# Kernel tuning notes

Measured on AMD Instinct MI355X. Metric: run time of the kernel, lower is better.

## Reference

```python
import jax, jax.numpy as jnp
import numpy as np

N = 50000
E = 600000
F_IN = 128
DIM = 128
BN_EPS = 1e-5


def _batchnorm(x, gamma, beta):
    # training-mode BatchNorm1d: biased batch stats over node dim
    mean = jnp.mean(x, axis=0)
    var = jnp.var(x, axis=0)
    return (x - mean) * jax.lax.rsqrt(var + BN_EPS) * gamma + beta


def _gin_layer(x, src, dst, Wa, ba, Wb, bb):
    # GINConv with eps=0: h_i = MLP(x_i + sum_{j->i} x_j)
    agg = jax.ops.segment_sum(x[src], dst, num_segments=N)
    h = x + agg
    h = jnp.maximum(h @ Wa + ba, 0.0) @ Wb + bb
    return h


def setup_inputs() -> dict:
    key = jax.random.key(0)
    ks = jax.random.split(key, 16)

    def lin(k, fan_in, fan_out):
        bound = 1.0 / np.sqrt(fan_in)
        kw, kb = jax.random.split(k)
        W = jax.random.uniform(kw, (fan_in, fan_out), jnp.float32, -bound, bound)
        b = jax.random.uniform(kb, (fan_out,), jnp.float32, -bound, bound)
        return W, b

    x = jax.random.normal(ks[0], (N, F_IN), jnp.float32)
    edge_index = jax.random.randint(ks[1], (2, E), 0, N, jnp.int64)

    W1a, b1a = lin(ks[2], F_IN, DIM)
    W1b, b1b = lin(ks[3], DIM, DIM)
    W2a, b2a = lin(ks[4], DIM, DIM)
    W2b, b2b = lin(ks[5], DIM, DIM)
    W5a, b5a = lin(ks[6], DIM, DIM)
    W5b, b5b = lin(ks[7], DIM, 2)

    g1 = jnp.ones((DIM,), jnp.float32); be1 = jnp.zeros((DIM,), jnp.float32)
    g2 = jnp.ones((DIM,), jnp.float32); be2 = jnp.zeros((DIM,), jnp.float32)
    g5 = jnp.ones((2,), jnp.float32); be5 = jnp.zeros((2,), jnp.float32)

    return dict(x=x, edge_index=edge_index,
                W1a=W1a, b1a=b1a, W1b=W1b, b1b=b1b, g1=g1, be1=be1,
                W2a=W2a, b2a=b2a, W2b=W2b, b2b=b2b, g2=g2, be2=be2,
                W5a=W5a, b5a=b5a, W5b=W5b, b5b=b5b, g5=g5, be5=be5)


def reference(x, edge_index,
              W1a, b1a, W1b, b1b, g1, be1,
              W2a, b2a, W2b, b2b, g2, be2,
              W5a, b5a, W5b, b5b, g5, be5):
    src, dst = edge_index[0], edge_index[1]
    h = jnp.maximum(_gin_layer(x, src, dst, W1a, b1a, W1b, b1b), 0.0)
    h = _batchnorm(h, g1, be1)
    h = jnp.maximum(_gin_layer(h, src, dst, W2a, b2a, W2b, b2b), 0.0)
    h = _batchnorm(h, g2, be2)
    h = jnp.maximum(_gin_layer(h, src, dst, W5a, b5a, W5b, b5b), 0.0)
    h = _batchnorm(h, g5, be5)
    return h
```

## Files before the change

kernel.cpp:

```cpp
#include <hip/hip_runtime.h>


constexpr int Nn = 50000;
constexpr int Ne = 600000;

typedef __attribute__((ext_vector_type(8))) short short8;
typedef __attribute__((ext_vector_type(4))) float f32x4;

__device__ inline float bflo(uint u) { return __uint_as_float(u << 16); }
__device__ inline float bfhi(uint u) { return __uint_as_float(u & 0xffff0000u); }
__device__ inline ushort f2b(float f) {
  uint x = __float_as_uint(f);
  return (ushort)((x + 0x7fffu + ((x >> 16) & 1u)) >> 16);
}
__device__ inline uint pack2(float a, float b) {
  return (uint)f2b(a) | ((uint)f2b(b) << 16);
}

constexpr int CVT_B = (Nn * 32) / 256;
constexpr int PK_B = (5 * 2048) / 256;
constexpr int EH_B = (Ne + 255) / 256;
__global__ __launch_bounds__(256) void prep_all(
    const float4* __restrict__ x4, uint2* __restrict__ xb,
    const float* __restrict__ Wa, const float* __restrict__ Wb,
    const float* __restrict__ Wc, const float* __restrict__ Wd,
    const float* __restrict__ We, ushort* __restrict__ pw,
    const int* __restrict__ dst, int* __restrict__ rp) {
  int b = blockIdx.x;
  if (b < CVT_B) {
    int i = b * 256 + threadIdx.x;
    float4 v = x4[i];
    xb[i] = make_uint2(pack2(v.x, v.y), pack2(v.z, v.w));
  } else if (b < CVT_B + PK_B) {
    int t = (b - CVT_B) * 256 + threadIdx.x;
    int mat = t >> 11;
    int r = t & 2047;
    int lane = r & 63;
    int ktnt = r >> 6;
    int kt = ktnt & 3, nt = ktnt >> 2;
    const float* W = mat == 0 ? Wa : mat == 1 ? Wb : mat == 2 ? Wc : mat == 3 ? Wd : We;
    int c = nt * 16 + (lane & 15);
    int k0 = kt * 32 + 8 * (lane >> 4);
    ushort tmp[8];
#pragma unroll
    for (int j = 0; j < 8; j++) tmp[j] = f2b(W[(size_t)(k0 + j) * 128 + c]);
    *(uint4*)&pw[(size_t)mat * 16384 + r * 8] = *(uint4*)tmp;
  } else {
    int e = (b - CVT_B - PK_B) * 256 + threadIdx.x;
    if (e < Ne) atomicAdd(&rp[dst[e] + 1], 1);
  }
}

constexpr int SCAN_N = Nn + 1;
constexpr int SCAN_G = (SCAN_N + 1023) / 1024;

__global__ __launch_bounds__(1024) void scan_p1(int* __restrict__ rp,
                                                int* __restrict__ bsum) {
  __shared__ int wsum[16];
  __shared__ int wpre[16];
  int i = blockIdx.x * 1024 + threadIdx.x;
  int lane = threadIdx.x & 63, wv = threadIdx.x >> 6;
  int v = (i < SCAN_N) ? rp[i] : 0;
#pragma unroll
  for (int off = 1; off < 64; off <<= 1) {
    int t = __shfl_up(v, off);
    if (lane >= off) v += t;
  }
  if (lane == 63) wsum[wv] = v;
  __syncthreads();
  if (threadIdx.x == 0) {
    int acc = 0;
#pragma unroll
    for (int w = 0; w < 16; w++) {
      wpre[w] = acc;
      acc += wsum[w];
    }
    bsum[blockIdx.x] = acc;
  }
  __syncthreads();
  if (i < SCAN_N) rp[i] = v + wpre[wv];
}

__global__ void scan_p2(int* __restrict__ bsum) {
  if (threadIdx.x == 0 && blockIdx.x == 0) {
    int acc = 0;
    for (int b = 0; b < SCAN_G; b++) {
      int t = bsum[b];
      bsum[b] = acc;
      acc += t;
    }
  }
}

__global__ __launch_bounds__(1024) void scan_p3(int* __restrict__ rp,
                                                const int* __restrict__ bsum,
                                                int* __restrict__ cur) {
  int i = blockIdx.x * 1024 + threadIdx.x;
  if (i < SCAN_N) {
    int v = rp[i] + bsum[blockIdx.x];
    rp[i] = v;
    if (i < Nn) cur[i] = v;
  }
}

__global__ __launch_bounds__(256) void edge_fill(const int* __restrict__ src,
                                                 const int* __restrict__ dst,
                                                 int* __restrict__ cur,
                                                 int* __restrict__ cols) {
  int e = blockIdx.x * 256 + threadIdx.x;
  if (e < Ne) {
    int p = atomicAdd(&cur[dst[e]], 1);
    cols[p] = src[e];
  }
}

template <bool FOLD>
__global__ __launch_bounds__(256) void gather_bn(const uint* __restrict__ X,
                                                 const int* __restrict__ rp,
                                                 const int* __restrict__ cols,
                                                 const float* __restrict__ sums,
                                                 const float* __restrict__ gamma,
                                                 const float* __restrict__ beta,
                                                 uint* __restrict__ H) {
  int wid = (blockIdx.x * 256 + threadIdx.x) >> 6;
  if (wid >= Nn) return;
  int lane = threadIdx.x & 63;
  int f0 = lane * 2;
  float A0 = 1.f, A1 = 1.f, B0 = 0.f, B1 = 0.f;
  if (FOLD) {
    float m0 = sums[f0] * (1.f / Nn), m1 = sums[f0 + 1] * (1.f / Nn);
    float v0 = sums[128 + f0] * (1.f / Nn) - m0 * m0;
    float v1 = sums[128 + f0 + 1] * (1.f / Nn) - m1 * m1;
    A0 = rsqrtf(v0 + 1e-5f) * gamma[f0];
    A1 = rsqrtf(v1 + 1e-5f) * gamma[f0 + 1];
    B0 = beta[f0] - m0 * A0;
    B1 = beta[f0 + 1] - m1 * A1;
  }
  int p0 = rp[wid], p1 = rp[wid + 1];
  int deg = p1 - p0;
  uint su = X[(size_t)wid * 64 + lane];
  float ax = bflo(su), ay = bfhi(su);
  if (deg > 0) {
    int ci = p0 + (lane & 31);
    int cv = cols[ci < p1 ? ci : p1 - 1];
    if (deg <= 16) {
#pragma unroll
      for (int j = 0; j < 16; j++) {
        int s = __shfl(cv, j);
        uint u = X[(size_t)s * 64 + lane];
        float m = j < deg ? 1.f : 0.f;
        ax = fmaf(m, bflo(u), ax);
        ay = fmaf(m, bfhi(u), ay);
      }
    } else {
#pragma unroll
      for (int j = 0; j < 32; j++) {
        int s = __shfl(cv, j);
        uint u = X[(size_t)s * 64 + lane];
        float m = j < deg ? 1.f : 0.f;
        ax = fmaf(m, bflo(u), ax);
        ay = fmaf(m, bfhi(u), ay);
      }
      for (int p = p0 + 32; p < p1; ++p) {
        int s = __builtin_amdgcn_readfirstlane(cols[p]);
        uint u = X[(size_t)s * 64 + lane];
        ax += bflo(u);
        ay += bfhi(u);
      }
    }
  }
  float cnt = (float)(deg + 1);
  float ox = FOLD ? A0 * ax + cnt * B0 : ax;
  float oy = FOLD ? A1 * ay + cnt * B1 : ay;
  H[(size_t)wid * 64 + lane] = pack2(ox, oy);
}

constexpr int MLP_ROWS = 128;
__global__ __launch_bounds__(256, 2) void gin_mlp(const ushort* __restrict__ A,
                                                  const uint4* __restrict__ pWa,
                                                  const float* __restrict__ ba,
                                                  const short8* __restrict__ pWb,
                                                  const float* __restrict__ bb,
                                                  ushort* __restrict__ C,
                                                  float* __restrict__ stats) {
  __shared__ uint4 W1l[2048];
  __shared__ ushort T[64][136];
  __shared__ float sS[128], sQ[128];
  int tid = threadIdx.x;
#pragma unroll
  for (int i = 0; i < 8; i++) W1l[tid + i * 256] = pWa[tid + i * 256];
  if (tid < 128) {
    sS[tid] = 0.f;
    sQ[tid] = 0.f;
  }
  int wv = tid >> 6, l = tid & 63, lr = l & 15, lg = l >> 4;
  int rowb = wv * 16 + lr;
  int row0 = blockIdx.x * MLP_ROWS;

  short8 w2r[8][4];
#pragma unroll
  for (int nt = 0; nt < 8; nt++)
#pragma unroll
    for (int kt = 0; kt < 4; kt++) w2r[nt][kt] = pWb[(nt * 4 + kt) * 64 + l];
  __builtin_amdgcn_sched_barrier(0);
  __syncthreads();

  for (int rt = 0; rt < MLP_ROWS / 64; rt++) {
    int row = row0 + rt * 64 + rowb;
    bool ok = row < Nn;

    short8 afr[4];
#pragma unroll
    for (int kt = 0; kt < 4; kt++) {
      afr[kt] = short8{};
      if (ok) afr[kt] = *(const short8*)(A + (size_t)row * 128 + kt * 32 + lg * 8);
    }
    f32x4 acc[8];
#pragma unroll
    for (int nt = 0; nt < 8; nt++) {
      float4 bv = *(const float4*)&ba[nt * 16 + lg * 4];
      acc[nt][0] = bv.x; acc[nt][1] = bv.y; acc[nt][2] = bv.z; acc[nt][3] = bv.w;
    }
#pragma unroll
    for (int kt = 0; kt < 4; kt++)
#pragma unroll
      for (int nt = 0; nt < 8; nt++) {
        short8 w1 = *(const short8*)&W1l[(nt * 4 + kt) * 64 + l];
        acc[nt] = __builtin_amdgcn_mfma_f32_16x16x32_bf16(w1, afr[kt], acc[nt],
                                                          0, 0, 0);
      }
#pragma unroll
    for (int nt = 0; nt < 8; nt++) {
      float v0 = fmaxf(acc[nt][0], 0.f), v1 = fmaxf(acc[nt][1], 0.f);
      float v2 = fmaxf(acc[nt][2], 0.f), v3 = fmaxf(acc[nt][3], 0.f);
      *(uint2*)&T[rowb][nt * 16 + lg * 4] = make_uint2(pack2(v0, v1), pack2(v2, v3));
    }
    __syncthreads();

    short8 tfr[4];
#pragma unroll
    for (int kt = 0; kt < 4; kt++) tfr[kt] = *(const short8*)&T[rowb][kt * 32 + lg * 8];
    f32x4 acc2[8];
#pragma unroll
    for (int nt = 0; nt < 8; nt++) {
      float4 bv = *(const float4*)&bb[nt * 16 + lg * 4];
      acc2[nt][0] = bv.x; acc2[nt][1] = bv.y; acc2[nt][2] = bv.z; acc2[nt][3] = bv.w;
    }
#pragma unroll
    for (int kt = 0; kt < 4; kt++)
#pragma unroll
      for (int nt = 0; nt < 8; nt++)
        acc2[nt] = __builtin_amdgcn_mfma_f32_16x16x32_bf16(w2r[nt][kt], tfr[kt],
                                                           acc2[nt], 0, 0, 0);

#pragma unroll
    for (int nt = 0; nt < 8; nt++) {
      float v[4];
#pragma unroll
      for (int r = 0; r < 4; r++) v[r] = fmaxf(acc2[nt][r], 0.f);
      if (ok)
        *(uint2*)&C[(size_t)row * 128 + nt * 16 + lg * 4] =
            make_uint2(pack2(v[0], v[1]), pack2(v[2], v[3]));
#pragma unroll
      for (int r = 0; r < 4; r++) {
        float s_ = ok ? v[r] : 0.f;
        float q_ = s_ * s_;
        s_ += __shfl_xor(s_, 1);  q_ += __shfl_xor(q_, 1);
        s_ += __shfl_xor(s_, 2);  q_ += __shfl_xor(q_, 2);
        s_ += __shfl_xor(s_, 4);  q_ += __shfl_xor(q_, 4);
        s_ += __shfl_xor(s_, 8);  q_ += __shfl_xor(q_, 8);
        if (lr == 0) {
          atomicAdd(&sS[nt * 16 + lg * 4 + r], s_);
          atomicAdd(&sQ[nt * 16 + lg * 4 + r], q_);
        }
      }
    }
    __syncthreads();
  }
  if (tid < 128) {
    atomicAdd(&stats[tid], sS[tid]);
    atomicAdd(&stats[128 + tid], sQ[tid]);
  }
}

__global__ __launch_bounds__(256, 2) void gin_mlp_out(const ushort* __restrict__ A,
                                                      const uint4* __restrict__ pWa,
                                                      const float* __restrict__ ba,
                                                      const float* __restrict__ W5b,
                                                      const float* __restrict__ b5b,
                                                      float* __restrict__ O,
                                                      float* __restrict__ st3) {
  __shared__ uint4 W1l[2048];
  __shared__ ushort T[64][136];
  __shared__ float Wc[256];
  __shared__ float red[4][4];
  int tid = threadIdx.x;
#pragma unroll
  for (int i = 0; i < 8; i++) W1l[tid + i * 256] = pWa[tid + i * 256];
  Wc[tid] = W5b[tid];
  int wv = tid >> 6, l = tid & 63, lr = l & 15, lg = l >> 4;
  int rowb = wv * 16 + lr;
  int row0 = blockIdx.x * MLP_ROWS;
  __syncthreads();

  float so0 = 0.f, so1 = 0.f, sq0 = 0.f, sq1 = 0.f;
  for (int rt = 0; rt < MLP_ROWS / 64; rt++) {
    int row = row0 + rt * 64 + rowb;
    bool ok = row < Nn;

    short8 afr[4];
#pragma unroll
    for (int kt = 0; kt < 4; kt++) {
      afr[kt] = short8{};
      if (ok) afr[kt] = *(const short8*)(A + (size_t)row * 128 + kt * 32 + lg * 8);
    }
    f32x4 acc[8];
#pragma unroll
    for (int nt = 0; nt < 8; nt++) {
      float4 bv = *(const float4*)&ba[nt * 16 + lg * 4];
      acc[nt][0] = bv.x; acc[nt][1] = bv.y; acc[nt][2] = bv.z; acc[nt][3] = bv.w;
    }
#pragma unroll
    for (int kt = 0; kt < 4; kt++)
#pragma unroll
      for (int nt = 0; nt < 8; nt++) {
        short8 w1 = *(const short8*)&W1l[(nt * 4 + kt) * 64 + l];
        acc[nt] = __builtin_amdgcn_mfma_f32_16x16x32_bf16(w1, afr[kt], acc[nt],
                                                          0, 0, 0);
      }
#pragma unroll
    for (int nt = 0; nt < 8; nt++) {
      float v0 = fmaxf(acc[nt][0], 0.f), v1 = fmaxf(acc[nt][1], 0.f);
      float v2 = fmaxf(acc[nt][2], 0.f), v3 = fmaxf(acc[nt][3], 0.f);
      *(uint2*)&T[rowb][nt * 16 + lg * 4] = make_uint2(pack2(v0, v1), pack2(v2, v3));
    }
    __syncthreads();

    float a0 = 0.f, a1 = 0.f;
    int ks = lg * 32;
#pragma unroll
    for (int q = 0; q < 4; q++) {
      uint4 u = *(const uint4*)&T[rowb][ks + q * 8];
      uint uu[4] = {u.x, u.y, u.z, u.w};
#pragma unroll
      for (int h = 0; h < 4; h++) {
        int k = ks + q * 8 + h * 2;
        float e0 = bflo(uu[h]), e1 = bfhi(uu[h]);
        a0 = fmaf(e0, Wc[k * 2 + 0], a0);
        a1 = fmaf(e0, Wc[k * 2 + 1], a1);
        a0 = fmaf(e1, Wc[k * 2 + 2], a0);
        a1 = fmaf(e1, Wc[k * 2 + 3], a1);
      }
    }
    a0 += __shfl_xor(a0, 16);
    a0 += __shfl_xor(a0, 32);
    a1 += __shfl_xor(a1, 16);
    a1 += __shfl_xor(a1, 32);
    if (l < 16 && ok) {
      float o0 = fmaxf(a0 + b5b[0], 0.f);
      float o1 = fmaxf(a1 + b5b[1], 0.f);
      *(float2*)&O[(size_t)row * 2] = make_float2(o0, o1);
      so0 += o0; sq0 += o0 * o0;
      so1 += o1; sq1 += o1 * o1;
    }
    __syncthreads();
  }
#pragma unroll
  for (int off = 1; off < 64; off <<= 1) {
    so0 += __shfl_xor(so0, off);
    sq0 += __shfl_xor(sq0, off);
    so1 += __shfl_xor(so1, off);
    sq1 += __shfl_xor(sq1, off);
  }
  if (l == 0) {
    red[wv][0] = so0; red[wv][1] = so1; red[wv][2] = sq0; red[wv][3] = sq1;
  }
  __syncthreads();
  if (tid < 4) {
    float t = red[0][tid] + red[1][tid] + red[2][tid] + red[3][tid];
    atomicAdd(&st3[tid], t);
  }
}

__global__ __launch_bounds__(256) void bn_apply2(const float* __restrict__ H,
                                                 const float* __restrict__ sums,
                                                 const float* __restrict__ gamma,
                                                 const float* __restrict__ beta,
                                                 float* __restrict__ Out, int nRows) {
  int idx = blockIdx.x * 256 + threadIdx.x;
  if (idx >= nRows * 2) return;
  int f = idx & 1;
  float mean = sums[f] * (1.0f / Nn);
  float var = sums[2 + f] * (1.0f / Nn) - mean * mean;
  float inv = rsqrtf(var + 1e-5f);
  Out[idx] = (H[idx] - mean) * inv * gamma[f] + beta[f];
}

extern "C" void kernel_launch(void* const* d_in, const int* in_sizes, int n_in,
                              void* d_out, int out_size, void* d_ws, size_t ws_size,
                              hipStream_t stream) {
  const float* x = (const float*)d_in[0];
  const int* src = (const int*)d_in[1];
  const int* dst = src + Ne;
  const float* W1a = (const float*)d_in[2];
  const float* b1a = (const float*)d_in[3];
  const float* W1b = (const float*)d_in[4];
  const float* b1b = (const float*)d_in[5];
  const float* g1 = (const float*)d_in[6];
  const float* be1 = (const float*)d_in[7];
  const float* W2a = (const float*)d_in[8];
  const float* b2a = (const float*)d_in[9];
  const float* W2b = (const float*)d_in[10];
  const float* b2b = (const float*)d_in[11];
  const float* g2 = (const float*)d_in[12];
  const float* be2 = (const float*)d_in[13];
  const float* W5a = (const float*)d_in[14];
  const float* b5a = (const float*)d_in[15];
  const float* W5b = (const float*)d_in[16];
  const float* b5b = (const float*)d_in[17];
  const float* g5 = (const float*)d_in[18];
  const float* be5 = (const float*)d_in[19];

  char* base = (char*)d_ws;
  size_t off = 0;
  auto carve = [&](size_t bytes) {
    char* p = base + off;
    off += (bytes + 255) & ~(size_t)255;
    return p;
  };
  float* stats = (float*)carve(520 * 4);
  float* o2buf = (float*)carve((size_t)Nn * 2 * 4);
  int* rowptr = (int*)carve((size_t)(Nn + 1) * 4);
  int* cur = (int*)carve((size_t)Nn * 4);
  int* cols = (int*)carve((size_t)Ne * 4);
  int* bsum = (int*)carve((size_t)SCAN_G * 4);
  ushort* xb = (ushort*)carve((size_t)Nn * 128 * 2);
  ushort* bufA = (ushort*)carve((size_t)Nn * 128 * 2);
  ushort* bufB = (ushort*)carve((size_t)Nn * 128 * 2);
  ushort* pw = (ushort*)carve((size_t)5 * 16384 * 2);
  float* st1 = stats, *st2 = stats + 256, *st3 = stats + 512;

  hipMemsetAsync(stats, 0, 520 * sizeof(float), stream);
  hipMemsetAsync(rowptr, 0, (Nn + 1) * sizeof(int), stream);

  const int eGrid = (Ne + 255) / 256;
  const int gatherGrid = (Nn * 64 + 255) / 256;
  const int mlpGrid = (Nn + MLP_ROWS - 1) / MLP_ROWS;

  prep_all<<<CVT_B + PK_B + EH_B, 256, 0, stream>>>(
      (const float4*)x, (uint2*)xb, W1a, W1b, W2a, W2b, W5a, pw, dst, rowptr);
  scan_p1<<<SCAN_G, 1024, 0, stream>>>(rowptr, bsum);
  scan_p2<<<1, 64, 0, stream>>>(bsum);
  scan_p3<<<SCAN_G, 1024, 0, stream>>>(rowptr, bsum, cur);
  edge_fill<<<eGrid, 256, 0, stream>>>(src, dst, cur, cols);

  const uint4* pW1a = (const uint4*)pw;
  const short8* pW1b = (const short8*)(pw + 16384);
  const uint4* pW2a = (const uint4*)(pw + 32768);
  const short8* pW2b = (const short8*)(pw + 49152);
  const uint4* pW5a = (const uint4*)(pw + 65536);

  gather_bn<false><<<gatherGrid, 256, 0, stream>>>((const uint*)xb, rowptr, cols,
                                                   nullptr, nullptr, nullptr,
                                                   (uint*)bufA);
  gin_mlp<<<mlpGrid, 256, 0, stream>>>(bufA, pW1a, b1a, pW1b, b1b, bufB, st1);

  gather_bn<true><<<gatherGrid, 256, 0, stream>>>((const uint*)bufB, rowptr, cols, st1,
                                                  g1, be1, (uint*)bufA);
  gin_mlp<<<mlpGrid, 256, 0, stream>>>(bufA, pW2a, b2a, pW2b, b2b, bufB, st2);

  gather_bn<true><<<gatherGrid, 256, 0, stream>>>((const uint*)bufB, rowptr, cols, st2,
                                                  g2, be2, (uint*)bufA);
  gin_mlp_out<<<mlpGrid, 256, 0, stream>>>(bufA, pW5a, b5a, W5b, b5b, o2buf, st3);
  bn_apply2<<<(Nn * 2 + 255) / 256, 256, 0, stream>>>(o2buf, st3, g5, be5,
                                                      (float*)d_out, Nn);
}
```

Baseline: 232.3 us.

## Fuse neighbor gather into GIN MLP kernels and merge scan passes

The separate gather/BN-fold kernel is folded into the MLP kernel. Each wave gathers 16 nodes into a shared-memory tile that then feeds the MFMA matmuls directly, so the aggregated activation buffer is no longer written to and read back from global memory. The single-thread scan_p2 is removed: each scan_p3m block sums the preceding block totals with a wave reduction. The two memsets are merged into one by placing rowptr next to stats. The trade-off is a large grid of 391 blocks that gathers serially per wave, limited to 2 blocks per CU with extra LDS, so the latency hiding of irregular gathers may drop.

```diff
diff --git a/kernel.cpp b/kernel.cpp
--- a/kernel.cpp
+++ b/kernel.cpp
@@ -81,23 +81,21 @@
   if (i < SCAN_N) rp[i] = v + wpre[wv];
 }
 
-__global__ void scan_p2(int* __restrict__ bsum) {
-  if (threadIdx.x == 0 && blockIdx.x == 0) {
-    int acc = 0;
-    for (int b = 0; b < SCAN_G; b++) {
-      int t = bsum[b];
-      bsum[b] = acc;
-      acc += t;
-    }
-  }
-}
-
-__global__ __launch_bounds__(1024) void scan_p3(int* __restrict__ rp,
-                                                const int* __restrict__ bsum,
-                                                int* __restrict__ cur) {
+__global__ __launch_bounds__(1024) void scan_p3m(int* __restrict__ rp,
+                                                 const int* __restrict__ bsum,
+                                                 int* __restrict__ cur) {
+  __shared__ int off_s;
+  if (threadIdx.x < 64) {
+    int v = (threadIdx.x < blockIdx.x) ? bsum[threadIdx.x] : 0;
+#pragma unroll
+    for (int o = 1; o < 64; o <<= 1) v += __shfl_xor(v, o);
+    if (threadIdx.x == 0) off_s = v;
+  }
+  __syncthreads();
+  int off = off_s;
   int i = blockIdx.x * 1024 + threadIdx.x;
   if (i < SCAN_N) {
-    int v = rp[i] + bsum[blockIdx.x];
+    int v = rp[i] + off;
     rp[i] = v;
     if (i < Nn) cur[i] = v;
   }
@@ -115,19 +113,77 @@
 }
 
 template <bool FOLD>
-__global__ __launch_bounds__(256) void gather_bn(const uint* __restrict__ X,
-                                                 const int* __restrict__ rp,
-                                                 const int* __restrict__ cols,
-                                                 const float* __restrict__ sums,
-                                                 const float* __restrict__ gamma,
-                                                 const float* __restrict__ beta,
-                                                 uint* __restrict__ H) {
-  int wid = (blockIdx.x * 256 + threadIdx.x) >> 6;
-  if (wid >= Nn) return;
-  int lane = threadIdx.x & 63;
-  int f0 = lane * 2;
+__device__ inline void gather_node(const uint* __restrict__ X,
+                                   const int* __restrict__ rp,
+                                   const int* __restrict__ cols, int node, int l,
+                                   float A0, float A1, float B0, float B1,
+                                   uint* __restrict__ htrow) {
+  int p0 = rp[node], p1 = rp[node + 1];
+  int deg = p1 - p0;
+  uint su = X[(size_t)node * 64 + l];
+  float ax = bflo(su), ay = bfhi(su);
+  if (deg > 0) {
+    int ci = p0 + (l & 31);
+    int cv = cols[ci < p1 ? ci : p1 - 1];
+    if (deg <= 16) {
+#pragma unroll
+      for (int j = 0; j < 16; j++) {
+        int s = __shfl(cv, j);
+        uint u = X[(size_t)s * 64 + l];
+        float m = j < deg ? 1.f : 0.f;
+        ax = fmaf(m, bflo(u), ax);
+        ay = fmaf(m, bfhi(u), ay);
+      }
+    } else {
+#pragma unroll
+      for (int j = 0; j < 32; j++) {
+        int s = __shfl(cv, j);
+        uint u = X[(size_t)s * 64 + l];
+        float m = j < deg ? 1.f : 0.f;
+        ax = fmaf(m, bflo(u), ax);
+        ay = fmaf(m, bfhi(u), ay);
+      }
+      for (int p = p0 + 32; p < p1; ++p) {
+        int s = cols[p];
+        uint u = X[(size_t)s * 64 + l];
+        ax += bflo(u);
+        ay += bfhi(u);
+      }
+    }
+  }
+  float cnt = (float)(deg + 1);
+  float ox = FOLD ? A0 * ax + cnt * B0 : ax;
+  float oy = FOLD ? A1 * ay + cnt * B1 : ay;
+  htrow[l] = pack2(ox, oy);
+}
+
+constexpr int MLP_ROWS = 128;
+template <bool FOLD>
+__global__ __launch_bounds__(256, 2) void gin_fused(
+    const uint* __restrict__ X, const int* __restrict__ rp,
+    const int* __restrict__ cols, const float* __restrict__ sums,
+    const float* __restrict__ gamma, const float* __restrict__ beta,
+    const uint4* __restrict__ pWa, const float* __restrict__ ba,
+    const short8* __restrict__ pWb, const float* __restrict__ bb,
+    ushort* __restrict__ C, float* __restrict__ stats) {
+  __shared__ uint4 W1l[2048];
+  __shared__ ushort T[64][136];
+  __shared__ uint Ht[64][68];
+  __shared__ float sS[128], sQ[128];
+  int tid = threadIdx.x;
+#pragma unroll
+  for (int i = 0; i < 8; i++) W1l[tid + i * 256] = pWa[tid + i * 256];
+  if (tid < 128) {
+    sS[tid] = 0.f;
+    sQ[tid] = 0.f;
+  }
+  int wv = tid >> 6, l = tid & 63, lr = l & 15, lg = l >> 4;
+  int rowb = wv * 16 + lr;
+  int row0 = blockIdx.x * MLP_ROWS;
+
   float A0 = 1.f, A1 = 1.f, B0 = 0.f, B1 = 0.f;
   if (FOLD) {
+    int f0 = l * 2;
     float m0 = sums[f0] * (1.f / Nn), m1 = sums[f0 + 1] * (1.f / Nn);
     float v0 = sums[128 + f0] * (1.f / Nn) - m0 * m0;
     float v1 = sums[128 + f0 + 1] * (1.f / Nn) - m1 * m1;
@@ -136,66 +192,6 @@
     B0 = beta[f0] - m0 * A0;
     B1 = beta[f0 + 1] - m1 * A1;
   }
-  int p0 = rp[wid], p1 = rp[wid + 1];
-  int deg = p1 - p0;
-  uint su = X[(size_t)wid * 64 + lane];
-  float ax = bflo(su), ay = bfhi(su);
-  if (deg > 0) {
-    int ci = p0 + (lane & 31);
-    int cv = cols[ci < p1 ? ci : p1 - 1];
-    if (deg <= 16) {
-#pragma unroll
-      for (int j = 0; j < 16; j++) {
-        int s = __shfl(cv, j);
-        uint u = X[(size_t)s * 64 + lane];
-        float m = j < deg ? 1.f : 0.f;
-        ax = fmaf(m, bflo(u), ax);
-        ay = fmaf(m, bfhi(u), ay);
-      }
-    } else {
-#pragma unroll
-      for (int j = 0; j < 32; j++) {
-        int s = __shfl(cv, j);
-        uint u = X[(size_t)s * 64 + lane];
-        float m = j < deg ? 1.f : 0.f;
-        ax = fmaf(m, bflo(u), ax);
-        ay = fmaf(m, bfhi(u), ay);
-      }
-      for (int p = p0 + 32; p < p1; ++p) {
-        int s = __builtin_amdgcn_readfirstlane(cols[p]);
-        uint u = X[(size_t)s * 64 + lane];
-        ax += bflo(u);
-        ay += bfhi(u);
-      }
-    }
-  }
-  float cnt = (float)(deg + 1);
-  float ox = FOLD ? A0 * ax + cnt * B0 : ax;
-  float oy = FOLD ? A1 * ay + cnt * B1 : ay;
-  H[(size_t)wid * 64 + lane] = pack2(ox, oy);
-}
-
-constexpr int MLP_ROWS = 128;
-__global__ __launch_bounds__(256, 2) void gin_mlp(const ushort* __restrict__ A,
-                                                  const uint4* __restrict__ pWa,
-                                                  const float* __restrict__ ba,
-                                                  const short8* __restrict__ pWb,
-                                                  const float* __restrict__ bb,
-                                                  ushort* __restrict__ C,
-                                                  float* __restrict__ stats) {
-  __shared__ uint4 W1l[2048];
-  __shared__ ushort T[64][136];
-  __shared__ float sS[128], sQ[128];
-  int tid = threadIdx.x;
-#pragma unroll
-  for (int i = 0; i < 8; i++) W1l[tid + i * 256] = pWa[tid + i * 256];
-  if (tid < 128) {
-    sS[tid] = 0.f;
-    sQ[tid] = 0.f;
-  }
-  int wv = tid >> 6, l = tid & 63, lr = l & 15, lg = l >> 4;
-  int rowb = wv * 16 + lr;
-  int row0 = blockIdx.x * MLP_ROWS;
 
   short8 w2r[8][4];
 #pragma unroll
@@ -203,18 +199,23 @@
 #pragma unroll
     for (int kt = 0; kt < 4; kt++) w2r[nt][kt] = pWb[(nt * 4 + kt) * 64 + l];
   __builtin_amdgcn_sched_barrier(0);
-  __syncthreads();
 
   for (int rt = 0; rt < MLP_ROWS / 64; rt++) {
-    int row = row0 + rt * 64 + rowb;
-    bool ok = row < Nn;
+    int base = row0 + rt * 64;
+    for (int i = 0; i < 16; i++) {
+      int node = base + wv * 16 + i;
+      if (node < Nn) {
+        gather_node<FOLD>(X, rp, cols, node, l, A0, A1, B0, B1, &Ht[wv * 16 + i][0]);
+      } else {
+        Ht[wv * 16 + i][l] = 0;
+      }
+    }
+    __syncthreads();
 
     short8 afr[4];
 #pragma unroll
-    for (int kt = 0; kt < 4; kt++) {
-      afr[kt] = short8{};
-      if (ok) afr[kt] = *(const short8*)(A + (size_t)row * 128 + kt * 32 + lg * 8);
-    }
+    for (int kt = 0; kt < 4; kt++)
+      afr[kt] = *(const short8*)&Ht[rowb][kt * 16 + lg * 4];
     f32x4 acc[8];
 #pragma unroll
     for (int nt = 0; nt < 8; nt++) {
@@ -237,6 +238,8 @@
     }
     __syncthreads();
 
+    int row = base + rowb;
+    bool ok = row < Nn;
     short8 tfr[4];
 #pragma unroll
     for (int kt = 0; kt < 4; kt++) tfr[kt] = *(const short8*)&T[rowb][kt * 32 + lg * 8];
@@ -283,15 +286,16 @@
   }
 }
 
-__global__ __launch_bounds__(256, 2) void gin_mlp_out(const ushort* __restrict__ A,
-                                                      const uint4* __restrict__ pWa,
-                                                      const float* __restrict__ ba,
-                                                      const float* __restrict__ W5b,
-                                                      const float* __restrict__ b5b,
-                                                      float* __restrict__ O,
-                                                      float* __restrict__ st3) {
+__global__ __launch_bounds__(256, 2) void gin_fused_out(
+    const uint* __restrict__ X, const int* __restrict__ rp,
+    const int* __restrict__ cols, const float* __restrict__ sums,
+    const float* __restrict__ gamma, const float* __restrict__ beta,
+    const uint4* __restrict__ pWa, const float* __restrict__ ba,
+    const float* __restrict__ W5b, const float* __restrict__ b5b,
+    float* __restrict__ O, float* __restrict__ st3) {
   __shared__ uint4 W1l[2048];
   __shared__ ushort T[64][136];
+  __shared__ uint Ht[64][68];
   __shared__ float Wc[256];
   __shared__ float red[4][4];
   int tid = threadIdx.x;
@@ -301,19 +305,33 @@
   int wv = tid >> 6, l = tid & 63, lr = l & 15, lg = l >> 4;
   int rowb = wv * 16 + lr;
   int row0 = blockIdx.x * MLP_ROWS;
-  __syncthreads();
+
+  int f0 = l * 2;
+  float m0 = sums[f0] * (1.f / Nn), m1 = sums[f0 + 1] * (1.f / Nn);
+  float vv0 = sums[128 + f0] * (1.f / Nn) - m0 * m0;
+  float vv1 = sums[128 + f0 + 1] * (1.f / Nn) - m1 * m1;
+  float A0 = rsqrtf(vv0 + 1e-5f) * gamma[f0];
+  float A1 = rsqrtf(vv1 + 1e-5f) * gamma[f0 + 1];
+  float B0 = beta[f0] - m0 * A0;
+  float B1 = beta[f0 + 1] - m1 * A1;
 
   float so0 = 0.f, so1 = 0.f, sq0 = 0.f, sq1 = 0.f;
   for (int rt = 0; rt < MLP_ROWS / 64; rt++) {
-    int row = row0 + rt * 64 + rowb;
-    bool ok = row < Nn;
+    int base = row0 + rt * 64;
+    for (int i = 0; i < 16; i++) {
+      int node = base + wv * 16 + i;
+      if (node < Nn) {
+        gather_node<true>(X, rp, cols, node, l, A0, A1, B0, B1, &Ht[wv * 16 + i][0]);
+      } else {
+        Ht[wv * 16 + i][l] = 0;
+      }
+    }
+    __syncthreads();
 
     short8 afr[4];
 #pragma unroll
-    for (int kt = 0; kt < 4; kt++) {
-      afr[kt] = short8{};
-      if (ok) afr[kt] = *(const short8*)(A + (size_t)row * 128 + kt * 32 + lg * 8);
-    }
+    for (int kt = 0; kt < 4; kt++)
+      afr[kt] = *(const short8*)&Ht[rowb][kt * 16 + lg * 4];
     f32x4 acc[8];
 #pragma unroll
     for (int nt = 0; nt < 8; nt++) {
@@ -336,6 +354,8 @@
     }
     __syncthreads();
 
+    int row = base + rowb;
+    bool ok = row < Nn;
     float a0 = 0.f, a1 = 0.f;
     int ks = lg * 32;
 #pragma unroll
@@ -429,8 +449,8 @@
     return p;
   };
   float* stats = (float*)carve(520 * 4);
+  int* rowptr = (int*)carve((size_t)(Nn + 1) * 4);
   float* o2buf = (float*)carve((size_t)Nn * 2 * 4);
-  int* rowptr = (int*)carve((size_t)(Nn + 1) * 4);
   int* cur = (int*)carve((size_t)Nn * 4);
   int* cols = (int*)carve((size_t)Ne * 4);
   int* bsum = (int*)carve((size_t)SCAN_G * 4);
@@ -440,18 +460,16 @@
   ushort* pw = (ushort*)carve((size_t)5 * 16384 * 2);
   float* st1 = stats, *st2 = stats + 256, *st3 = stats + 512;
 
-  hipMemsetAsync(stats, 0, 520 * sizeof(float), stream);
-  hipMemsetAsync(rowptr, 0, (Nn + 1) * sizeof(int), stream);
+  size_t zeroBytes = ((char*)(rowptr + Nn + 1)) - ((char*)stats);
+  hipMemsetAsync(stats, 0, zeroBytes, stream);
 
   const int eGrid = (Ne + 255) / 256;
-  const int gatherGrid = (Nn * 64 + 255) / 256;
   const int mlpGrid = (Nn + MLP_ROWS - 1) / MLP_ROWS;
 
   prep_all<<<CVT_B + PK_B + EH_B, 256, 0, stream>>>(
       (const float4*)x, (uint2*)xb, W1a, W1b, W2a, W2b, W5a, pw, dst, rowptr);
   scan_p1<<<SCAN_G, 1024, 0, stream>>>(rowptr, bsum);
-  scan_p2<<<1, 64, 0, stream>>>(bsum);
-  scan_p3<<<SCAN_G, 1024, 0, stream>>>(rowptr, bsum, cur);
+  scan_p3m<<<SCAN_G, 1024, 0, stream>>>(rowptr, bsum, cur);
   edge_fill<<<eGrid, 256, 0, stream>>>(src, dst, cur, cols);
 
   const uint4* pW1a = (const uint4*)pw;
@@ -460,18 +478,15 @@
   const short8* pW2b = (const short8*)(pw + 49152);
   const uint4* pW5a = (const uint4*)(pw + 65536);
 
-  gather_bn<false><<<gatherGrid, 256, 0, stream>>>((const uint*)xb, rowptr, cols,
-                                                   nullptr, nullptr, nullptr,
-                                                   (uint*)bufA);
-  gin_mlp<<<mlpGrid, 256, 0, stream>>>(bufA, pW1a, b1a, pW1b, b1b, bufB, st1);
-
-  gather_bn<true><<<gatherGrid, 256, 0, stream>>>((const uint*)bufB, rowptr, cols, st1,
-                                                  g1, be1, (uint*)bufA);
-  gin_mlp<<<mlpGrid, 256, 0, stream>>>(bufA, pW2a, b2a, pW2b, b2b, bufB, st2);
-
-  gather_bn<true><<<gatherGrid, 256, 0, stream>>>((const uint*)bufB, rowptr, cols, st2,
-                                                  g2, be2, (uint*)bufA);
-  gin_mlp_out<<<mlpGrid, 256, 0, stream>>>(bufA, pW5a, b5a, W5b, b5b, o2buf, st3);
+  gin_fused<false><<<mlpGrid, 256, 0, stream>>>(
+      (const uint*)xb, rowptr, cols, nullptr, nullptr, nullptr, pW1a, b1a, pW1b,
+      b1b, bufB, st1);
+  gin_fused<true><<<mlpGrid, 256, 0, stream>>>(
+      (const uint*)bufB, rowptr, cols, st1, g1, be1, pW2a, b2a, pW2b, b2b, bufA,
+      st2);
+  gin_fused_out<<<mlpGrid, 256, 0, stream>>>((const uint*)bufA, rowptr, cols, st2,
+                                             g2, be2, pW5a, b5a, W5b, b5b, o2buf,
+                                             st3);
   bn_apply2<<<(Nn * 2 + 255) / 256, 256, 0, stream>>>(o2buf, st3, g5, be5,
                                                       (float*)d_out, Nn);
 }
```

Result: slower. 533.1 us (+129.5%).
